# Optimization experiments

Measured on AMD Instinct MI355X. Metric: run time of the kernel, lower is better.

## Reference

```python
import jax, jax.numpy as jnp
import numpy as np

N, E, D, L, H = 10000, 160000, 128, 3, 8
DH = D // H
EPS = 1e-5


def ln(x, g, b):
    m = x.mean(-1, keepdims=True)
    v = ((x - m) ** 2).mean(-1, keepdims=True)
    return (x - m) * jax.lax.rsqrt(v + EPS) * g + b


def setup_inputs() -> dict:
    key = jax.random.key(0)
    ks = iter(jax.random.split(key, 16))
    rn = lambda s, sc=0.05: jax.random.normal(next(ks), s, dtype=jnp.float32) * sc
    return {
        'lane_feats': jax.random.normal(next(ks), (N, 10), dtype=jnp.float32),
        'edge_attrs': jax.random.normal(next(ks), (E, 9), dtype=jnp.float32),
        'edge_index': jax.random.randint(next(ks), (2, E), 0, N),
        'node_W': rn((10, D)), 'node_b': jnp.zeros((D,)), 'node_g': jnp.ones((D,)), 'node_bt': jnp.zeros((D,)),
        'rpe_W': rn((9, D)), 'rpe_b': jnp.zeros((D,)), 'rpe_g': jnp.ones((D,)), 'rpe_bt': jnp.zeros((D,)),
        'mem_W': rn((L, 3 * D, D)), 'mem_b': jnp.zeros((L, D)), 'mem_g': jnp.ones((L, D)), 'mem_bt': jnp.zeros((L, D)),
        'Wq': rn((L, D, D)), 'Wk': rn((L, D, D)), 'Wv': rn((L, D, D)), 'Wo': rn((L, D, D)),
        'eu_W': rn((L, D, D)), 'eu_b': jnp.zeros((L, D)), 'eu_g': jnp.ones((L, D)), 'eu_bt': jnp.zeros((L, D)),
        'en_g': jnp.ones((L, D)), 'en_bt': jnp.zeros((L, D)),
        'ffn_W1': rn((L, D, 2 * D)), 'ffn_b1': jnp.zeros((L, 2 * D)),
        'ffn_W2': rn((L, 2 * D, D)), 'ffn_b2': jnp.zeros((L, D)),
        'n1_g': jnp.ones((L, D)), 'n1_bt': jnp.zeros((L, D)),
        'n2_g': jnp.ones((L, D)), 'n2_bt': jnp.zeros((L, D)),
    }


def reference(lane_feats, edge_attrs, edge_index,
              node_W, node_b, node_g, node_bt,
              rpe_W, rpe_b, rpe_g, rpe_bt,
              mem_W, mem_b, mem_g, mem_bt,
              Wq, Wk, Wv, Wo,
              eu_W, eu_b, eu_g, eu_bt,
              en_g, en_bt,
              ffn_W1, ffn_b1, ffn_W2, ffn_b2,
              n1_g, n1_bt, n2_g, n2_bt):
    src, dst = edge_index[0], edge_index[1]
    # input projections (dropout is identity in eval)
    x = jax.nn.relu(ln(lane_feats @ node_W + node_b, node_g, node_bt))  # [N, D]
    e = jax.nn.relu(ln(edge_attrs @ rpe_W + rpe_b, rpe_g, rpe_bt))      # [E, D]
    for l in range(L):
        x_i, x_j = x[dst], x[src]  # receiver / sender features [E, D]
        mem = jax.nn.relu(ln(jnp.concatenate([x_i, x_j, e], axis=-1) @ mem_W[l] + mem_b[l],
                             mem_g[l], mem_bt[l]))
        delta = jax.nn.relu(ln(mem @ eu_W[l] + eu_b[l], eu_g[l], eu_bt[l]))
        e = ln(e + delta, en_g[l], en_bt[l])
        q = (x_i @ Wq[l]).reshape(E, H, DH)
        k = (mem @ Wk[l]).reshape(E, H, DH)
        v = (mem @ Wv[l]).reshape(E, H, DH)
        logits = (q * k).sum(-1) / np.float32(np.sqrt(DH))  # [E, H]
        # segment softmax over destination nodes (pyg_softmax)
        mx = jax.ops.segment_max(logits, dst, num_segments=N)
        ex = jnp.exp(logits - mx[dst])
        sm = jax.ops.segment_sum(ex, dst, num_segments=N)
        attn = ex / (sm[dst] + 1e-16)
        out_e = (attn[..., None] * v).reshape(E, D) @ Wo[l]
        agg = jax.ops.segment_sum(out_e, dst, num_segments=N)  # scatter-add aggregation
        x = ln(x + agg, n1_g[l], n1_bt[l])
        h = jax.nn.relu(x @ ffn_W1[l] + ffn_b1[l]) @ ffn_W2[l] + ffn_b2[l]
        x = ln(x + h, n2_g[l], n2_bt[l])
    return x
```

## Files before the change

kernel.cpp:

```cpp
#include <hip/hip_runtime.h>
#include <cstdint>

#define NN 10000
#define NE 160000
#define DD 128
#define NL 3

typedef __attribute__((ext_vector_type(8))) __bf16 bf16x8;
typedef __attribute__((ext_vector_type(4))) float f32x4;

__device__ __forceinline__ ushort f2bf(float f) {
  unsigned u = __float_as_uint(f);
  return (ushort)((u + 0x7fffu + ((u >> 16) & 1u)) >> 16);
}
__device__ __forceinline__ float bf2f(ushort s) {
  return __uint_as_float(((unsigned)s) << 16);
}
__device__ __forceinline__ float wsum32(float v) {
  v += __shfl_xor(v, 1); v += __shfl_xor(v, 2); v += __shfl_xor(v, 4);
  v += __shfl_xor(v, 8); v += __shfl_xor(v, 16);
  return v;
}
__device__ __forceinline__ float wsum64(float v) {
  v = wsum32(v); v += __shfl_xor(v, 32); return v;
}
__device__ __forceinline__ void red16_2(float& a, float& b) {
#pragma unroll
  for (int m = 1; m < 16; m <<= 1) { a += __shfl_xor(a, m); b += __shfl_xor(b, m); }
}
__device__ __forceinline__ uint4 ldg16(const ushort* p) { return *(const uint4*)p; }

#define PH(id, MAXID, AT, ASTR, KK, AS) {                                       \
    if ((id) < (MAXID)) {                                                       \
      ushort* _db = Bb[((id) + 1) & 1];                                         \
      if ((id) & 1) { *(uint4*)(_db + tid * 8) = sa0;                           \
                      *(uint4*)(_db + 2048 + tid * 8) = sa1; }                  \
      else          { *(uint4*)(_db + tid * 8) = sb0;                           \
                      *(uint4*)(_db + 2048 + tid * 8) = sb1; }                  \
    }                                                                           \
    if ((id) + 2 <= (MAXID)) {                                                  \
      if ((id) & 1) { sb0 = ldg16(csrc((id) + 2, tid));                         \
                      sb1 = ldg16(csrc((id) + 2, 256 + tid)); }                 \
      else          { sa0 = ldg16(csrc((id) + 2, tid));                         \
                      sa1 = ldg16(csrc((id) + 2, 256 + tid)); }                 \
    }                                                                           \
    { bf16x8 _a = *(const bf16x8*)((AT) + (r0 + c) * (ASTR) + (KK) * 32 + g * 8); \
      const ushort* _bp = Bb[(id) & 1] + lane * 8;                              \
      _Pragma("unroll") for (int _t = 0; _t < 8; ++_t)                          \
        AS[_t] = __builtin_amdgcn_mfma_f32_16x16x32_bf16(                       \
            _a, *(const bf16x8*)(_bp + _t * 512), AS[_t], 0, 0, 0); }           \
    __syncthreads(); }

__global__ __launch_bounds__(256) void k_hist(const int* __restrict__ dst,
                                              int* __restrict__ deg) {
  int e = blockIdx.x * 256 + threadIdx.x;
  if (e < NE) atomicAdd(&deg[dst[e]], 1);
}

__global__ __launch_bounds__(256) void k_scan(const int* __restrict__ deg,
                                              int* __restrict__ rowptr,
                                              int* __restrict__ cursor) {
  __shared__ int part[256];
  const int t = threadIdx.x;
  const int CH = 40;
  int base = t * CH;
  int s = 0;
  for (int i = 0; i < CH; ++i) {
    int idx = base + i;
    s += (idx < NN) ? deg[idx] : 0;
  }
  part[t] = s;
  __syncthreads();
  for (int off = 1; off < 256; off <<= 1) {
    int v = (t >= off) ? part[t - off] : 0;
    __syncthreads();
    part[t] += v;
    __syncthreads();
  }
  int run = (t == 0) ? 0 : part[t - 1];
  for (int i = 0; i < CH; ++i) {
    int idx = base + i;
    if (idx < NN) {
      rowptr[idx] = run;
      cursor[idx] = run;
      run += deg[idx];
    }
  }
  if (t == 255) rowptr[NN] = part[255];
}

__global__ __launch_bounds__(256) void k_scatter(const int* __restrict__ dst,
                                                 int* __restrict__ cursor,
                                                 int* __restrict__ eids) {
  int e = blockIdx.x * 256 + threadIdx.x;
  if (e < NE) {
    int pos = atomicAdd(&cursor[dst[e]], 1);
    eids[pos] = e;
  }
}

__global__ __launch_bounds__(256) void k_permidx(const int* __restrict__ ei,
                                                 const int* __restrict__ perm,
                                                 int* __restrict__ srcP,
                                                 int* __restrict__ dstP) {
  int i = blockIdx.x * 256 + threadIdx.x;
  if (i < NE) {
    int e = perm[i];
    srcP[i] = ei[e];
    dstP[i] = ei[NE + e];
  }
}

__global__ __launch_bounds__(256) void k_transp(const float* __restrict__ in,
                                                ushort* __restrict__ out,
                                                int K, int N) {
  __shared__ float T[32][33];
  int k0 = blockIdx.x * 32, n0 = blockIdx.y * 32;
  in += (size_t)blockIdx.z * K * N;
  out += (size_t)blockIdx.z * K * N;
  int tx = threadIdx.x & 31, ty = threadIdx.x >> 5;
#pragma unroll
  for (int r = 0; r < 32; r += 8)
    if (k0 + ty + r < K && n0 + tx < N)
      T[ty + r][tx] = in[(size_t)(k0 + ty + r) * N + n0 + tx];
  __syncthreads();
#pragma unroll
  for (int r = 0; r < 32; r += 8)
    if (n0 + ty + r < N && k0 + tx < K)
      out[(size_t)(n0 + ty + r) * K + k0 + tx] = f2bf(T[tx][ty + r]);
}

template <int K>
__global__ __launch_bounds__(256) void k_inproj(
    const float* __restrict__ inp, const int* __restrict__ perm,
    const float* __restrict__ W, const float* __restrict__ b,
    const float* __restrict__ g, const float* __restrict__ bt,
    float* __restrict__ outF, ushort* __restrict__ outB, int rows) {
  int row = blockIdx.x * 4 + (threadIdx.x >> 6);
  if (row >= rows) return;
  int srow = perm ? perm[row] : row;
  int lane = threadIdx.x & 63;
  float a0 = b[lane], a1 = b[lane + 64];
#pragma unroll
  for (int k = 0; k < K; ++k) {
    float xv = inp[(size_t)srow * K + k];
    a0 = fmaf(xv, W[k * DD + lane], a0);
    a1 = fmaf(xv, W[k * DD + lane + 64], a1);
  }
  float m = wsum64(a0 + a1) * (1.0f / DD);
  float q = wsum64(a0 * a0 + a1 * a1) * (1.0f / DD);
  float rstd = rsqrtf(q - m * m + 1e-5f);
  float o0 = fmaxf((a0 - m) * rstd * g[lane] + bt[lane], 0.0f);
  float o1 = fmaxf((a1 - m) * rstd * g[lane + 64] + bt[lane + 64], 0.0f);
  size_t base = (size_t)row * DD;
  if (outF) { outF[base + lane] = o0; outF[base + lane + 64] = o1; }
  outB[base + lane] = f2bf(o0);
  outB[base + lane + 64] = f2bf(o1);
}

__global__ __launch_bounds__(256) void k_nodepre(
    const ushort* __restrict__ xb, const ushort* __restrict__ memWT,
    const ushort* __restrict__ WqT, const float* __restrict__ memB,
    float* __restrict__ Pa, float* __restrict__ Pb, ushort* __restrict__ qbo) {
  __shared__ __align__(16) ushort Xt[64 * 136];
  __shared__ __align__(16) ushort Bb[4096];
  const int tid = threadIdx.x;
  const int n0 = blockIdx.x * 64;
  const int z = blockIdx.y;
  const ushort* B0 = (z == 0) ? memWT : ((z == 1) ? memWT + 128 : WqT);
  const int bstr = (z < 2) ? 384 : 128;
  uint4 w[2], wn[2];
#pragma unroll
  for (int i = 0; i < 2; ++i) {
    int u = tid + i * 256;
    w[i] = ldg16(B0 + (size_t)(u >> 2) * bstr + (u & 3) * 8);
  }
#pragma unroll
  for (int it = 0; it < 4; ++it) {
    int ch = it * 256 + tid, row = ch >> 4, j = ch & 15;
    int gr = n0 + row; if (gr > NN - 1) gr = NN - 1;
    *(uint4*)(Xt + row * 136 + j * 8) = *(const uint4*)(xb + (size_t)gr * DD + j * 8);
  }
  const int lane = tid & 63, wv = tid >> 6;
  const int c = lane & 15, g = lane >> 4, r0 = wv * 16;
  f32x4 acc[8];
#pragma unroll
  for (int t = 0; t < 8; ++t) acc[t] = (f32x4){0.f, 0.f, 0.f, 0.f};
#pragma unroll
  for (int kk = 0; kk < 4; ++kk) {
    __syncthreads();
#pragma unroll
    for (int i = 0; i < 2; ++i) *(uint4*)(Bb + (tid + i * 256) * 8) = w[i];
    if (kk < 3) {
#pragma unroll
      for (int i = 0; i < 2; ++i) {
        int u = tid + i * 256;
        wn[i] = ldg16(B0 + (size_t)(u >> 2) * bstr + (kk + 1) * 32 + (u & 3) * 8);
      }
    }
    __syncthreads();
    bf16x8 a = *(const bf16x8*)(Xt + (r0 + c) * 136 + kk * 32 + g * 8);
#pragma unroll
    for (int t = 0; t < 8; ++t)
      acc[t] = __builtin_amdgcn_mfma_f32_16x16x32_bf16(
          a, *(const bf16x8*)(Bb + (t * 16 + c) * 32 + g * 8), acc[t], 0, 0, 0);
#pragma unroll
    for (int i = 0; i < 2; ++i) w[i] = wn[i];
  }
  if (z == 0) {
#pragma unroll
    for (int t = 0; t < 8; ++t) {
      float bv = memB[t * 16 + c];
#pragma unroll
      for (int rr = 0; rr < 4; ++rr) {
        int row = n0 + r0 + g * 4 + rr;
        if (row < NN) Pa[(size_t)row * DD + t * 16 + c] = acc[t][rr] + bv;
      }
    }
  } else if (z == 1) {
#pragma unroll
    for (int t = 0; t < 8; ++t)
#pragma unroll
      for (int rr = 0; rr < 4; ++rr) {
        int row = n0 + r0 + g * 4 + rr;
        if (row < NN) Pb[(size_t)row * DD + t * 16 + c] = acc[t][rr];
      }
  } else {
#pragma unroll
    for (int t = 0; t < 8; ++t)
#pragma unroll
      for (int rr = 0; rr < 4; ++rr) {
        int row = n0 + r0 + g * 4 + rr;
        if (row < NN) qbo[(size_t)row * DD + t * 16 + c] = f2bf(acc[t][rr]);
      }
  }
}

__global__ __launch_bounds__(256) void k_edge(
    ushort* __restrict__ ebg, ushort* __restrict__ vbg,
    const float* __restrict__ Pa, const float* __restrict__ Pb,
    const ushort* __restrict__ qb, const int* __restrict__ srcP,
    const int* __restrict__ dstP, const ushort* __restrict__ memWT,
    const float* __restrict__ memG, const float* __restrict__ memBt,
    const ushort* __restrict__ euWT, const float* __restrict__ euB,
    const float* __restrict__ euG, const float* __restrict__ euBt,
    const float* __restrict__ enG, const float* __restrict__ enBt,
    const ushort* __restrict__ WkT, const ushort* __restrict__ WvT,
    float* __restrict__ lg) {
  __shared__ __align__(16) ushort Et[64 * 136];
  __shared__ __align__(16) ushort Mt[64 * 136];
  __shared__ __align__(16) ushort Pt[64 * 136];
  __shared__ __align__(16) ushort Bb[2][4096];
  __shared__ int sD[64], sS[64];
  const int tid = threadIdx.x;
  const int e0 = blockIdx.x * 64;

  auto csrc = [&](int j, int u) -> const ushort* {
    const ushort* base; int stride, off, kk = j & 3;
    if (j < 4)       { base = memWT; stride = 384; off = 256 + kk * 32; }
    else if (j < 8)  { base = euWT;  stride = 128; off = kk * 32; }
    else if (j < 12) { base = WkT;   stride = 128; off = kk * 32; }
    else             { base = WvT;   stride = 128; off = kk * 32; }
    return base + ((u >> 6) * 16 + (u & 15)) * stride + off + ((u >> 4) & 3) * 8;
  };

  if (tid < 64) { sS[tid] = srcP[e0 + tid]; sD[tid] = dstP[e0 + tid]; }
  uint4 sa0 = ldg16(csrc(0, tid)), sa1 = ldg16(csrc(0, 256 + tid));
  uint4 sb0 = ldg16(csrc(1, tid)), sb1 = ldg16(csrc(1, 256 + tid));
  __syncthreads();
#pragma unroll
  for (int it = 0; it < 4; ++it) {
    int ch = it * 256 + tid, row = ch >> 4, j = ch & 15;
    *(uint4*)(Et + row * 136 + j * 8) =
        *(const uint4*)(ebg + (size_t)(e0 + row) * DD + j * 8);
  }
#pragma unroll
  for (int it = 0; it < 8; ++it) {
    int u = it * 256 + tid, row = u >> 5, j = u & 31;
    float4 va = *(const float4*)(Pa + (size_t)sD[row] * DD + j * 4);
    float4 vb = *(const float4*)(Pb + (size_t)sS[row] * DD + j * 4);
    ushort4 o;
    o.x = f2bf(va.x + vb.x); o.y = f2bf(va.y + vb.y);
    o.z = f2bf(va.z + vb.z); o.w = f2bf(va.w + vb.w);
    *(ushort4*)(Pt + row * 136 + j * 4) = o;
  }
  *(uint4*)(Bb[0] + tid * 8) = sa0;
  *(uint4*)(Bb[0] + 2048 + tid * 8) = sa1;
  __syncthreads();

  const int lane = tid & 63, wv = tid >> 6;
  const int c = lane & 15, g = lane >> 4, r0 = wv * 16;
  f32x4 acc[8];

#pragma unroll
  for (int t = 0; t < 8; ++t) acc[t] = (f32x4){0.f, 0.f, 0.f, 0.f};
  PH(0, 15, Et, 136, 0, acc)
  PH(1, 15, Et, 136, 1, acc)
  PH(2, 15, Et, 136, 2, acc)
  PH(3, 15, Et, 136, 3, acc)

  {
    float s1[4] = {0, 0, 0, 0}, s2[4] = {0, 0, 0, 0};
#pragma unroll
    for (int t = 0; t < 8; ++t)
#pragma unroll
      for (int rr = 0; rr < 4; ++rr) {
        float pv = bf2f(Pt[(r0 + g * 4 + rr) * 136 + t * 16 + c]);
        float s = acc[t][rr] + pv;
        acc[t][rr] = s; s1[rr] += s; s2[rr] += s * s;
      }
    float mean[4], rstd[4];
#pragma unroll
    for (int rr = 0; rr < 4; ++rr) {
      red16_2(s1[rr], s2[rr]);
      mean[rr] = s1[rr] * (1.f / DD);
      rstd[rr] = rsqrtf(s2[rr] * (1.f / DD) - mean[rr] * mean[rr] + 1e-5f);
    }
#pragma unroll
    for (int t = 0; t < 8; ++t) {
      float gv = memG[t * 16 + c], tv = memBt[t * 16 + c];
#pragma unroll
      for (int rr = 0; rr < 4; ++rr) {
        float o = fmaxf((acc[t][rr] - mean[rr]) * rstd[rr] * gv + tv, 0.f);
        Mt[(r0 + g * 4 + rr) * 136 + t * 16 + c] = f2bf(o);
      }
    }
  }
  __syncthreads();

  uint4 q0 = ldg16(qb + (size_t)sD[tid >> 4] * DD + (tid & 15) * 8);
  uint4 q1 = ldg16(qb + (size_t)sD[(256 + tid) >> 4] * DD + (tid & 15) * 8);
  uint4 q2 = ldg16(qb + (size_t)sD[(512 + tid) >> 4] * DD + (tid & 15) * 8);
  uint4 q3 = ldg16(qb + (size_t)sD[(768 + tid) >> 4] * DD + (tid & 15) * 8);

#pragma unroll
  for (int t = 0; t < 8; ++t) acc[t] = (f32x4){0.f, 0.f, 0.f, 0.f};
  PH(4, 15, Mt, 136, 0, acc)
  PH(5, 15, Mt, 136, 1, acc)
  {
    *(uint4*)(Pt + (tid >> 4) * 136 + (tid & 15) * 8) = q0;
    *(uint4*)(Pt + ((256 + tid) >> 4) * 136 + (tid & 15) * 8) = q1;
    *(uint4*)(Pt + ((512 + tid) >> 4) * 136 + (tid & 15) * 8) = q2;
    *(uint4*)(Pt + ((768 + tid) >> 4) * 136 + (tid & 15) * 8) = q3;
  }
  PH(6, 15, Mt, 136, 2, acc)
  PH(7, 15, Mt, 136, 3, acc)

  {
    float s1[4] = {0, 0, 0, 0}, s2[4] = {0, 0, 0, 0};
#pragma unroll
    for (int t = 0; t < 8; ++t) {
      float bv = euB[t * 16 + c];
#pragma unroll
      for (int rr = 0; rr < 4; ++rr) {
        float v2 = acc[t][rr] + bv;
        acc[t][rr] = v2; s1[rr] += v2; s2[rr] += v2 * v2;
      }
    }
    float mean[4], rstd[4];
#pragma unroll
    for (int rr = 0; rr < 4; ++rr) {
      red16_2(s1[rr], s2[rr]);
      mean[rr] = s1[rr] * (1.f / DD);
      rstd[rr] = rsqrtf(s2[rr] * (1.f / DD) - mean[rr] * mean[rr] + 1e-5f);
    }
    float t1[4] = {0, 0, 0, 0}, t2[4] = {0, 0, 0, 0};
#pragma unroll
    for (int t = 0; t < 8; ++t) {
      float gv = euG[t * 16 + c], tv = euBt[t * 16 + c];
#pragma unroll
      for (int rr = 0; rr < 4; ++rr) {
        float d = fmaxf((acc[t][rr] - mean[rr]) * rstd[rr] * gv + tv, 0.f);
        float eo = bf2f(Et[(r0 + g * 4 + rr) * 136 + t * 16 + c]);
        float pv = eo + d;
        acc[t][rr] = pv; t1[rr] += pv; t2[rr] += pv * pv;
      }
    }
    float mean3[4], rstd3[4];
#pragma unroll
    for (int rr = 0; rr < 4; ++rr) {
      red16_2(t1[rr], t2[rr]);
      mean3[rr] = t1[rr] * (1.f / DD);
      rstd3[rr] = rsqrtf(t2[rr] * (1.f / DD) - mean3[rr] * mean3[rr] + 1e-5f);
    }
#pragma unroll
    for (int t = 0; t < 8; ++t) {
      float gv = enG[t * 16 + c], tv = enBt[t * 16 + c];
#pragma unroll
      for (int rr = 0; rr < 4; ++rr) {
        float en = (acc[t][rr] - mean3[rr]) * rstd3[rr] * gv + tv;
        Et[(r0 + g * 4 + rr) * 136 + t * 16 + c] = f2bf(en);
      }
    }
  }
  __syncthreads();
#pragma unroll
  for (int it = 0; it < 4; ++it) {
    int ch = it * 256 + tid, row = ch >> 4, j = ch & 15;
    *(uint4*)(ebg + (size_t)(e0 + row) * DD + j * 8) =
        *(const uint4*)(Et + row * 136 + j * 8);
  }

#pragma unroll
  for (int t = 0; t < 8; ++t) acc[t] = (f32x4){0.f, 0.f, 0.f, 0.f};
  PH(8, 15, Mt, 136, 0, acc)
  PH(9, 15, Mt, 136, 1, acc)
  PH(10, 15, Mt, 136, 2, acc)
  PH(11, 15, Mt, 136, 3, acc)
#pragma unroll
  for (int t = 0; t < 8; ++t) {
    float p[4];
#pragma unroll
    for (int rr = 0; rr < 4; ++rr)
      p[rr] = acc[t][rr] * bf2f(Pt[(r0 + g * 4 + rr) * 136 + t * 16 + c]);
#pragma unroll
    for (int m = 1; m < 16; m <<= 1)
#pragma unroll
      for (int rr = 0; rr < 4; ++rr) p[rr] += __shfl_xor(p[rr], m);
    if (c == t) {
#pragma unroll
      for (int rr = 0; rr < 4; ++rr)
        lg[(size_t)(e0 + r0 + g * 4 + rr) * 8 + t] = p[rr] * 0.25f;
    }
  }

#pragma unroll
  for (int t = 0; t < 8; ++t) acc[t] = (f32x4){0.f, 0.f, 0.f, 0.f};
  PH(12, 15, Mt, 136, 0, acc)
  PH(13, 15, Mt, 136, 1, acc)
  PH(14, 15, Mt, 136, 2, acc)
  PH(15, 15, Mt, 136, 3, acc)
#pragma unroll
  for (int t = 0; t < 8; ++t)
#pragma unroll
    for (int rr = 0; rr < 4; ++rr)
      Et[(r0 + g * 4 + rr) * 136 + t * 16 + c] = f2bf(acc[t][rr]);
  __syncthreads();
#pragma unroll
  for (int it = 0; it < 4; ++it) {
    int ch = it * 256 + tid, row = ch >> 4, j = ch & 15;
    *(uint4*)(vbg + (size_t)(e0 + row) * DD + j * 8) =
        *(const uint4*)(Et + row * 136 + j * 8);
  }
}

__global__ __launch_bounds__(256) void k_aggr(
    const ushort* __restrict__ vbg, const float* __restrict__ lg,
    const int* __restrict__ rowptr, float* __restrict__ agg) {
  int node = blockIdx.x * 4 + (threadIdx.x >> 6);
  if (node >= NN) return;
  const int lane = threadIdx.x & 63;
  const int j = lane & 7, h = lane >> 3;
  const int beg = rowptr[node], end = rowptr[node + 1];
  float mx = -3.4e38f;
  for (int i = beg + j; i < end; i += 8)
    mx = fmaxf(mx, lg[(size_t)i * 8 + h]);
  mx = fmaxf(mx, __shfl_xor(mx, 1));
  mx = fmaxf(mx, __shfl_xor(mx, 2));
  mx = fmaxf(mx, __shfl_xor(mx, 4));
  float sm = 0.f;
  for (int i = beg + j; i < end; i += 8)
    sm += expf(lg[(size_t)i * 8 + h] - mx);
  sm += __shfl_xor(sm, 1);
  sm += __shfl_xor(sm, 2);
  sm += __shfl_xor(sm, 4);
  float inv = 1.f / (sm + 1e-16f);
  float acc0 = 0.f, acc1 = 0.f;
  for (int i = beg; i < end; ++i) {
    float w = expf(lg[(size_t)i * 8 + h] - mx) * inv;
    ushort2 vv = *(const ushort2*)(vbg + (size_t)i * DD + lane * 2);
    acc0 = fmaf(bf2f(vv.x), w, acc0);
    acc1 = fmaf(bf2f(vv.y), w, acc1);
  }
  *(float2*)(agg + (size_t)node * DD + lane * 2) = make_float2(acc0, acc1);
}

__global__ __launch_bounds__(256) void k_node2(
    const float* __restrict__ vagg, const ushort* __restrict__ WoT,
    const float* __restrict__ xres_g, const float* __restrict__ g1,
    const float* __restrict__ bt1, const ushort* __restrict__ W1T,
    const float* __restrict__ b1, const ushort* __restrict__ W2T,
    const float* __restrict__ b2, const float* __restrict__ g2,
    const float* __restrict__ bt2, float* __restrict__ out,
    ushort* __restrict__ outB) {
  __shared__ __align__(16) ushort Xt[64 * 136];
  __shared__ __align__(16) ushort Hs[64 * 264];
  __shared__ __align__(16) ushort Bb[8192];
  const int tid = threadIdx.x;
  const int n0 = blockIdx.x * 64;
  const int lane = tid & 63, wv = tid >> 6;
  const int c = lane & 15, g = lane >> 4, r0 = wv * 16;

  float xres[8][4];
#pragma unroll
  for (int t = 0; t < 8; ++t)
#pragma unroll
    for (int rr = 0; rr < 4; ++rr) {
      int row = n0 + r0 + g * 4 + rr;
      if (row > NN - 1) row = NN - 1;
      xres[t][rr] = xres_g[(size_t)row * DD + t * 16 + c];
    }
  uint4 w[4], wn[4];
#pragma unroll
  for (int i = 0; i < 2; ++i) {
    int u = tid + i * 256;
    w[i] = ldg16(WoT + (size_t)(u >> 2) * 128 + (u & 3) * 8);
  }
#pragma unroll
  for (int it = 0; it < 8; ++it) {
    int ch = it * 256 + tid, row = ch >> 5, j = ch & 31;
    int gr = n0 + row; if (gr > NN - 1) gr = NN - 1;
    float4 vv = *(const float4*)(vagg + (size_t)gr * DD + j * 4);
    ushort4 ov; ov.x = f2bf(vv.x); ov.y = f2bf(vv.y); ov.z = f2bf(vv.z); ov.w = f2bf(vv.w);
    *(ushort4*)(Xt + row * 136 + j * 4) = ov;
  }
  f32x4 acc0[8];
#pragma unroll
  for (int t = 0; t < 8; ++t) acc0[t] = (f32x4){0.f, 0.f, 0.f, 0.f};
#pragma unroll
  for (int kk = 0; kk < 4; ++kk) {
    __syncthreads();
#pragma unroll
    for (int i = 0; i < 2; ++i) *(uint4*)(Bb + (tid + i * 256) * 8) = w[i];
    if (kk < 3) {
#pragma unroll
      for (int i = 0; i < 2; ++i) {
        int u = tid + i * 256;
        wn[i] = ldg16(WoT + (size_t)(u >> 2) * 128 + (kk + 1) * 32 + (u & 3) * 8);
      }
    }
    __syncthreads();
    bf16x8 a = *(const bf16x8*)(Xt + (r0 + c) * 136 + kk * 32 + g * 8);
#pragma unroll
    for (int t = 0; t < 8; ++t)
      acc0[t] = __builtin_amdgcn_mfma_f32_16x16x32_bf16(
          a, *(const bf16x8*)(Bb + (t * 16 + c) * 32 + g * 8), acc0[t], 0, 0, 0);
#pragma unroll
    for (int i = 0; i < 2; ++i) w[i] = wn[i];
  }
  {
    float s1[4] = {0, 0, 0, 0}, s2[4] = {0, 0, 0, 0};
#pragma unroll
    for (int t = 0; t < 8; ++t)
#pragma unroll
      for (int rr = 0; rr < 4; ++rr) {
        float s = acc0[t][rr] + xres[t][rr];
        acc0[t][rr] = s; s1[rr] += s; s2[rr] += s * s;
      }
    float mean[4], rstd[4];
#pragma unroll
    for (int rr = 0; rr < 4; ++rr) {
      red16_2(s1[rr], s2[rr]);
      mean[rr] = s1[rr] * (1.f / DD);
      rstd[rr] = rsqrtf(s2[rr] * (1.f / DD) - mean[rr] * mean[rr] + 1e-5f);
    }
#pragma unroll
    for (int t = 0; t < 8; ++t) {
      float gv = g1[t * 16 + c], tv = bt1[t * 16 + c];
#pragma unroll
      for (int rr = 0; rr < 4; ++rr) {
        float o = (acc0[t][rr] - mean[rr]) * rstd[rr] * gv + tv;
        Xt[(r0 + g * 4 + rr) * 136 + t * 16 + c] = f2bf(o);
      }
    }
  }
  f32x4 acc16[16];
#pragma unroll
  for (int t = 0; t < 16; ++t) acc16[t] = (f32x4){0.f, 0.f, 0.f, 0.f};
#pragma unroll
  for (int i = 0; i < 4; ++i) {
    int u = tid + i * 256;
    w[i] = ldg16(W1T + (size_t)(u >> 2) * 128 + (u & 3) * 8);
  }
#pragma unroll
  for (int kk = 0; kk < 4; ++kk) {
    __syncthreads();
#pragma unroll
    for (int i = 0; i < 4; ++i) *(uint4*)(Bb + (tid + i * 256) * 8) = w[i];
    if (kk < 3) {
#pragma unroll
      for (int i = 0; i < 4; ++i) {
        int u = tid + i * 256;
        wn[i] = ldg16(W1T + (size_t)(u >> 2) * 128 + (kk + 1) * 32 + (u & 3) * 8);
      }
    }
    __syncthreads();
    bf16x8 a = *(const bf16x8*)(Xt + (r0 + c) * 136 + kk * 32 + g * 8);
#pragma unroll
    for (int t = 0; t < 16; ++t)
      acc16[t] = __builtin_amdgcn_mfma_f32_16x16x32_bf16(
          a, *(const bf16x8*)(Bb + (t * 16 + c) * 32 + g * 8), acc16[t], 0, 0, 0);
#pragma unroll
    for (int i = 0; i < 4; ++i) w[i] = wn[i];
  }
#pragma unroll
  for (int t = 0; t < 16; ++t) {
    float bv = b1[t * 16 + c];
#pragma unroll
    for (int rr = 0; rr < 4; ++rr)
      Hs[(r0 + g * 4 + rr) * 264 + t * 16 + c] = f2bf(fmaxf(acc16[t][rr] + bv, 0.f));
  }
#pragma unroll
  for (int t = 0; t < 8; ++t) acc0[t] = (f32x4){0.f, 0.f, 0.f, 0.f};
#pragma unroll
  for (int i = 0; i < 2; ++i) {
    int u = tid + i * 256;
    w[i] = ldg16(W2T + (size_t)(u >> 2) * 256 + (u & 3) * 8);
  }
#pragma unroll
  for (int kk = 0; kk < 8; ++kk) {
    __syncthreads();
#pragma unroll
    for (int i = 0; i < 2; ++i) *(uint4*)(Bb + (tid + i * 256) * 8) = w[i];
    if (kk < 7) {
#pragma unroll
      for (int i = 0; i < 2; ++i) {
        int u = tid + i * 256;
        wn[i] = ldg16(W2T + (size_t)(u >> 2) * 256 + (kk + 1) * 32 + (u & 3) * 8);
      }
    }
    __syncthreads();
    bf16x8 a = *(const bf16x8*)(Hs + (r0 + c) * 264 + kk * 32 + g * 8);
#pragma unroll
    for (int t = 0; t < 8; ++t)
      acc0[t] = __builtin_amdgcn_mfma_f32_16x16x32_bf16(
          a, *(const bf16x8*)(Bb + (t * 16 + c) * 32 + g * 8), acc0[t], 0, 0, 0);
#pragma unroll
    for (int i = 0; i < 2; ++i) w[i] = wn[i];
  }
  {
    float s1[4] = {0, 0, 0, 0}, s2[4] = {0, 0, 0, 0};
#pragma unroll
    for (int t = 0; t < 8; ++t) {
      float bv = b2[t * 16 + c];
#pragma unroll
      for (int rr = 0; rr < 4; ++rr) {
        float s = acc0[t][rr] + bv + bf2f(Xt[(r0 + g * 4 + rr) * 136 + t * 16 + c]);
        acc0[t][rr] = s; s1[rr] += s; s2[rr] += s * s;
      }
    }
    float mean[4], rstd[4];
#pragma unroll
    for (int rr = 0; rr < 4; ++rr) {
      red16_2(s1[rr], s2[rr]);
      mean[rr] = s1[rr] * (1.f / DD);
      rstd[rr] = rsqrtf(s2[rr] * (1.f / DD) - mean[rr] * mean[rr] + 1e-5f);
    }
#pragma unroll
    for (int t = 0; t < 8; ++t) {
      float gv = g2[t * 16 + c], tv = bt2[t * 16 + c];
#pragma unroll
      for (int rr = 0; rr < 4; ++rr) {
        float o = (acc0[t][rr] - mean[rr]) * rstd[rr] * gv + tv;
        int row = n0 + r0 + g * 4 + rr;
        if (row < NN) out[(size_t)row * DD + t * 16 + c] = o;
        Xt[(r0 + g * 4 + rr) * 136 + t * 16 + c] = f2bf(o);
      }
    }
  }
  __syncthreads();
#pragma unroll
  for (int it = 0; it < 4; ++it) {
    int ch = it * 256 + tid, row = ch >> 4, j = ch & 15;
    int gr = n0 + row;
    if (gr < NN)
      *(uint4*)(outB + (size_t)gr * DD + j * 8) = *(const uint4*)(Xt + row * 136 + j * 8);
  }
}

extern "C" void kernel_launch(void* const* d_in, const int* in_sizes, int n_in,
                              void* d_out, int out_size, void* d_ws,
                              size_t ws_size, hipStream_t stream) {
  (void)in_sizes; (void)n_in; (void)out_size; (void)ws_size;
  const float* lane_feats = (const float*)d_in[0];
  const float* edge_attrs = (const float*)d_in[1];
  const int* ei = (const int*)d_in[2];
  const int* dst = ei + NE;
  const float* node_W = (const float*)d_in[3];
  const float* node_b = (const float*)d_in[4];
  const float* node_g = (const float*)d_in[5];
  const float* node_bt = (const float*)d_in[6];
  const float* rpe_W = (const float*)d_in[7];
  const float* rpe_b = (const float*)d_in[8];
  const float* rpe_g = (const float*)d_in[9];
  const float* rpe_bt = (const float*)d_in[10];
  const float* mem_W = (const float*)d_in[11];
  const float* mem_b = (const float*)d_in[12];
  const float* mem_g = (const float*)d_in[13];
  const float* mem_bt = (const float*)d_in[14];
  const float* Wq = (const float*)d_in[15];
  const float* Wk = (const float*)d_in[16];
  const float* Wv = (const float*)d_in[17];
  const float* Wo = (const float*)d_in[18];
  const float* eu_W = (const float*)d_in[19];
  const float* eu_b = (const float*)d_in[20];
  const float* eu_g = (const float*)d_in[21];
  const float* eu_bt = (const float*)d_in[22];
  const float* en_g = (const float*)d_in[23];
  const float* en_bt = (const float*)d_in[24];
  const float* ffn_W1 = (const float*)d_in[25];
  const float* ffn_b1 = (const float*)d_in[26];
  const float* ffn_W2 = (const float*)d_in[27];
  const float* ffn_b2 = (const float*)d_in[28];
  const float* n1_g = (const float*)d_in[29];
  const float* n1_bt = (const float*)d_in[30];
  const float* n2_g = (const float*)d_in[31];
  const float* n2_bt = (const float*)d_in[32];

  char* p = (char*)d_ws;
  auto alloc = [&](size_t bytes) -> char* {
    char* r = p; p += (bytes + 255) & ~(size_t)255; return r;
  };
  float* x = (float*)alloc((size_t)NN * DD * 4);
  float* vagg = (float*)alloc((size_t)NN * DD * 4);
  float* lg = (float*)alloc((size_t)NE * 8 * 4);
  float* Pa = (float*)alloc((size_t)NN * DD * 4);
  float* Pb = (float*)alloc((size_t)NN * DD * 4);
  ushort* qb = (ushort*)alloc((size_t)NN * DD * 2);
  ushort* xb = (ushort*)alloc((size_t)NN * DD * 2);
  ushort* eb = (ushort*)alloc((size_t)NE * DD * 2);
  ushort* vb = (ushort*)alloc((size_t)NE * DD * 2);
  ushort* memWT = (ushort*)alloc((size_t)NL * DD * 384 * 2);
  ushort* euWT = (ushort*)alloc((size_t)NL * DD * DD * 2);
  ushort* WqT = (ushort*)alloc((size_t)NL * DD * DD * 2);
  ushort* WkT = (ushort*)alloc((size_t)NL * DD * DD * 2);
  ushort* WvT = (ushort*)alloc((size_t)NL * DD * DD * 2);
  ushort* WoT = (ushort*)alloc((size_t)NL * DD * DD * 2);
  ushort* W1T = (ushort*)alloc((size_t)NL * 256 * DD * 2);
  ushort* W2T = (ushort*)alloc((size_t)NL * DD * 256 * 2);
  int* deg = (int*)alloc((size_t)NN * 4);
  int* rowptr = (int*)alloc((size_t)(NN + 1) * 4);
  int* cursor = (int*)alloc((size_t)NN * 4);
  int* eids = (int*)alloc((size_t)NE * 4);
  int* srcP = (int*)alloc((size_t)NE * 4);
  int* dstP = (int*)alloc((size_t)NE * 4);

  hipMemsetAsync(deg, 0, (size_t)NN * 4, stream);
  k_hist<<<NE / 256, 256, 0, stream>>>(dst, deg);
  k_scan<<<1, 256, 0, stream>>>(deg, rowptr, cursor);
  k_scatter<<<NE / 256, 256, 0, stream>>>(dst, cursor, eids);
  k_permidx<<<NE / 256, 256, 0, stream>>>(ei, eids, srcP, dstP);

  k_transp<<<dim3(12, 4, NL), 256, 0, stream>>>(mem_W, memWT, 384, DD);
  k_transp<<<dim3(4, 4, NL), 256, 0, stream>>>(eu_W, euWT, DD, DD);
  k_transp<<<dim3(4, 4, NL), 256, 0, stream>>>(Wq, WqT, DD, DD);
  k_transp<<<dim3(4, 4, NL), 256, 0, stream>>>(Wk, WkT, DD, DD);
  k_transp<<<dim3(4, 4, NL), 256, 0, stream>>>(Wv, WvT, DD, DD);
  k_transp<<<dim3(4, 4, NL), 256, 0, stream>>>(Wo, WoT, DD, DD);
  k_transp<<<dim3(4, 8, NL), 256, 0, stream>>>(ffn_W1, W1T, DD, 256);
  k_transp<<<dim3(8, 4, NL), 256, 0, stream>>>(ffn_W2, W2T, 256, DD);

  k_inproj<10><<<NN / 4, 256, 0, stream>>>(lane_feats, nullptr, node_W, node_b,
                                           node_g, node_bt, x, xb, NN);
  k_inproj<9><<<NE / 4, 256, 0, stream>>>(edge_attrs, eids, rpe_W, rpe_b,
                                          rpe_g, rpe_bt, nullptr, eb, NE);

  const int NB = (NN + 63) / 64;
  for (int l = 0; l < NL; ++l) {
    k_nodepre<<<dim3(NB, 3), 256, 0, stream>>>(
        xb, memWT + (size_t)l * DD * 384, WqT + (size_t)l * DD * DD,
        mem_b + l * DD, Pa, Pb, qb);
    k_edge<<<NE / 64, 256, 0, stream>>>(
        eb, vb, Pa, Pb, qb, srcP, dstP, memWT + (size_t)l * DD * 384,
        mem_g + l * DD, mem_bt + l * DD, euWT + (size_t)l * DD * DD,
        eu_b + l * DD, eu_g + l * DD, eu_bt + l * DD, en_g + l * DD,
        en_bt + l * DD, WkT + (size_t)l * DD * DD, WvT + (size_t)l * DD * DD,
        lg);
    k_aggr<<<(NN + 3) / 4, 256, 0, stream>>>(vb, lg, rowptr, vagg);
    k_node2<<<NB, 256, 0, stream>>>(
        vagg, WoT + (size_t)l * DD * DD, x, n1_g + l * DD, n1_bt + l * DD,
        W1T + (size_t)l * 256 * DD, ffn_b1 + l * 256,
        W2T + (size_t)l * DD * 256, ffn_b2 + l * DD, n2_g + l * DD,
        n2_bt + l * DD, (l == NL - 1) ? (float*)d_out : x, xb);
  }
}
```

Measured before the change: 559.1 us.

## Drop Pt shared tile; gather node projections and q directly into registers

Removes the Pt shared-memory staging buffer and the sD/sS index arrays. Each thread now loads its own edge indices and gathers Pa+Pb and q values straight from global memory in the MFMA accumulator layout, which drops a barrier and about 17KB of LDS per block. A launch bound of 3 blocks per SM is added to raise occupancy. The cost is scalar 4-byte and 2-byte gathers that coalesce poorly compared with the old 16-byte vector loads, more register pressure from the held values, and less overlap of the q loads with the MFMA work.

```diff
diff --git a/kernel.cpp b/kernel.cpp
--- a/kernel.cpp
+++ b/kernel.cpp
@@ -236,7 +236,7 @@
   }
 }
 
-__global__ __launch_bounds__(256) void k_edge(
+__global__ __launch_bounds__(256, 3) void k_edge(
     ushort* __restrict__ ebg, ushort* __restrict__ vbg,
     const float* __restrict__ Pa, const float* __restrict__ Pb,
     const ushort* __restrict__ qb, const int* __restrict__ srcP,
@@ -249,11 +249,11 @@
     float* __restrict__ lg) {
   __shared__ __align__(16) ushort Et[64 * 136];
   __shared__ __align__(16) ushort Mt[64 * 136];
-  __shared__ __align__(16) ushort Pt[64 * 136];
   __shared__ __align__(16) ushort Bb[2][4096];
-  __shared__ int sD[64], sS[64];
   const int tid = threadIdx.x;
   const int e0 = blockIdx.x * 64;
+  const int lane = tid & 63, wv = tid >> 6;
+  const int c = lane & 15, g = lane >> 4, r0 = wv * 16;
 
   auto csrc = [&](int j, int u) -> const ushort* {
     const ushort* base; int stride, off, kk = j & 3;
@@ -264,32 +264,24 @@
     return base + ((u >> 6) * 16 + (u & 15)) * stride + off + ((u >> 4) & 3) * 8;
   };
 
-  if (tid < 64) { sS[tid] = srcP[e0 + tid]; sD[tid] = dstP[e0 + tid]; }
+  int dv[4], sv[4];
+#pragma unroll
+  for (int rr = 0; rr < 4; ++rr) {
+    int row = e0 + r0 + g * 4 + rr;
+    dv[rr] = dstP[row]; sv[rr] = srcP[row];
+  }
   uint4 sa0 = ldg16(csrc(0, tid)), sa1 = ldg16(csrc(0, 256 + tid));
   uint4 sb0 = ldg16(csrc(1, tid)), sb1 = ldg16(csrc(1, 256 + tid));
-  __syncthreads();
 #pragma unroll
   for (int it = 0; it < 4; ++it) {
     int ch = it * 256 + tid, row = ch >> 4, j = ch & 15;
     *(uint4*)(Et + row * 136 + j * 8) =
         *(const uint4*)(ebg + (size_t)(e0 + row) * DD + j * 8);
   }
-#pragma unroll
-  for (int it = 0; it < 8; ++it) {
-    int u = it * 256 + tid, row = u >> 5, j = u & 31;
-    float4 va = *(const float4*)(Pa + (size_t)sD[row] * DD + j * 4);
-    float4 vb = *(const float4*)(Pb + (size_t)sS[row] * DD + j * 4);
-    ushort4 o;
-    o.x = f2bf(va.x + vb.x); o.y = f2bf(va.y + vb.y);
-    o.z = f2bf(va.z + vb.z); o.w = f2bf(va.w + vb.w);
-    *(ushort4*)(Pt + row * 136 + j * 4) = o;
-  }
   *(uint4*)(Bb[0] + tid * 8) = sa0;
   *(uint4*)(Bb[0] + 2048 + tid * 8) = sa1;
   __syncthreads();
 
-  const int lane = tid & 63, wv = tid >> 6;
-  const int c = lane & 15, g = lane >> 4, r0 = wv * 16;
   f32x4 acc[8];
 
 #pragma unroll
@@ -300,13 +292,19 @@
   PH(3, 15, Et, 136, 3, acc)
 
   {
+    float ps[8][4];
+#pragma unroll
+    for (int t = 0; t < 8; ++t)
+#pragma unroll
+      for (int rr = 0; rr < 4; ++rr)
+        ps[t][rr] = Pa[(size_t)dv[rr] * DD + t * 16 + c] +
+                    Pb[(size_t)sv[rr] * DD + t * 16 + c];
     float s1[4] = {0, 0, 0, 0}, s2[4] = {0, 0, 0, 0};
 #pragma unroll
     for (int t = 0; t < 8; ++t)
 #pragma unroll
       for (int rr = 0; rr < 4; ++rr) {
-        float pv = bf2f(Pt[(r0 + g * 4 + rr) * 136 + t * 16 + c]);
-        float s = acc[t][rr] + pv;
+        float s = acc[t][rr] + ps[t][rr];
         acc[t][rr] = s; s1[rr] += s; s2[rr] += s * s;
       }
     float mean[4], rstd[4];
@@ -328,21 +326,10 @@
   }
   __syncthreads();
 
-  uint4 q0 = ldg16(qb + (size_t)sD[tid >> 4] * DD + (tid & 15) * 8);
-  uint4 q1 = ldg16(qb + (size_t)sD[(256 + tid) >> 4] * DD + (tid & 15) * 8);
-  uint4 q2 = ldg16(qb + (size_t)sD[(512 + tid) >> 4] * DD + (tid & 15) * 8);
-  uint4 q3 = ldg16(qb + (size_t)sD[(768 + tid) >> 4] * DD + (tid & 15) * 8);
-
 #pragma unroll
   for (int t = 0; t < 8; ++t) acc[t] = (f32x4){0.f, 0.f, 0.f, 0.f};
   PH(4, 15, Mt, 136, 0, acc)
   PH(5, 15, Mt, 136, 1, acc)
-  {
-    *(uint4*)(Pt + (tid >> 4) * 136 + (tid & 15) * 8) = q0;
-    *(uint4*)(Pt + ((256 + tid) >> 4) * 136 + (tid & 15) * 8) = q1;
-    *(uint4*)(Pt + ((512 + tid) >> 4) * 136 + (tid & 15) * 8) = q2;
-    *(uint4*)(Pt + ((768 + tid) >> 4) * 136 + (tid & 15) * 8) = q3;
-  }
   PH(6, 15, Mt, 136, 2, acc)
   PH(7, 15, Mt, 136, 3, acc)
 
@@ -400,6 +387,13 @@
     *(uint4*)(ebg + (size_t)(e0 + row) * DD + j * 8) =
         *(const uint4*)(Et + row * 136 + j * 8);
   }
+
+  float qvf[8][4];
+#pragma unroll
+  for (int t = 0; t < 8; ++t)
+#pragma unroll
+    for (int rr = 0; rr < 4; ++rr)
+      qvf[t][rr] = bf2f(qb[(size_t)dv[rr] * DD + t * 16 + c]);
 
 #pragma unroll
   for (int t = 0; t < 8; ++t) acc[t] = (f32x4){0.f, 0.f, 0.f, 0.f};
@@ -411,8 +405,7 @@
   for (int t = 0; t < 8; ++t) {
     float p[4];
 #pragma unroll
-    for (int rr = 0; rr < 4; ++rr)
-      p[rr] = acc[t][rr] * bf2f(Pt[(r0 + g * 4 + rr) * 136 + t * 16 + c]);
+    for (int rr = 0; rr < 4; ++rr) p[rr] = acc[t][rr] * qvf[t][rr];
 #pragma unroll
     for (int m = 1; m < 16; m <<= 1)
 #pragma unroll
```

Result: faster. 522.3 us (-6.6%).
